# Optimization experiments

Measured on AMD Instinct MI355X. Metric: run time of the kernel, lower is better.

Reference implementation:

```python
import jax, jax.numpy as jnp
import numpy as np

SEQ_LEN = 2048
EMB = 512
BATCH = 8


def _xavier_uniform(key, shape):
    fan_in, fan_out = shape[0], shape[1]
    bound = float(np.sqrt(6.0 / (fan_in + fan_out)))
    return jax.random.uniform(key, shape, dtype=jnp.float32, minval=-bound, maxval=bound)


def setup_inputs() -> dict:
    key = jax.random.key(0)
    kx, k1, k2 = jax.random.split(key, 3)
    x = jax.random.normal(kx, (BATCH, EMB, SEQ_LEN), dtype=jnp.float32)
    weight1 = _xavier_uniform(k1, (EMB, EMB))
    weight2 = _xavier_uniform(k2, (EMB, EMB))
    return {"x": x, "weight1": weight1, "weight2": weight2}


def reference(x, weight1, weight2):
    # x: [b, e, s]
    s = x.shape[-1]
    # projections: O(b*s*e^2)
    fitnesses1 = jnp.einsum('bes,ef->bfs', x, weight1)   # [b, e, s]
    fitnesses2 = jnp.einsum('bfs,ef->bes', x, weight2)   # [b, e, s]
    # s x t interaction matrix: O(b*s^2*e)
    weight = jnp.einsum('bes,bet->bst', fitnesses1, fitnesses2)  # [b, s, t]
    # zero strictly-upper triangle (t > s), as in torch.triu(..., diagonal=1)
    mask = jnp.triu(jnp.ones((s, s), dtype=bool), k=1)
    weight = jnp.where(mask, jnp.zeros((), dtype=weight.dtype), weight)
    fitnesses = jnp.einsum('bst,bet->bes', weight, x)    # [b, e, s]
    avg_fitness = jnp.einsum('bes,bes->be', x, fitnesses)[..., None]  # [b, e, 1]
    net_fitnesses = fitnesses - avg_fitness
    x_next = x + x * net_fitnesses
    return jax.nn.relu(x_next)
```

## Files before the change

### kernel.cpp

```cpp
#include <hip/hip_runtime.h>
#include <hip/hip_bf16.h>
#include <stdint.h>


#define SEQ 2048
#define EMB 512
#define NBATCH 8

typedef unsigned short u16;
typedef __bf16 bf16x8 __attribute__((ext_vector_type(8)));
typedef float f32x4 __attribute__((ext_vector_type(4)));
typedef u16 u16x8 __attribute__((ext_vector_type(8)));

#define AS1 __attribute__((address_space(1)))
#define AS3 __attribute__((address_space(3)))

#define SBAR do { __builtin_amdgcn_sched_barrier(0); __builtin_amdgcn_s_barrier(); \
                  __builtin_amdgcn_sched_barrier(0); } while (0)
#define LGKM0 do { asm volatile("s_waitcnt lgkmcnt(0)" ::: "memory"); \
                   __builtin_amdgcn_sched_barrier(0); } while (0)

__device__ __forceinline__ u16 f2bf(float f) {
  uint32_t u = __builtin_bit_cast(uint32_t, f);
  uint32_t r = u + 0x7FFFu + ((u >> 16) & 1u);
  return (u16)(r >> 16);
}
__device__ __forceinline__ float bf2f(u16 u) {
  return __builtin_bit_cast(float, (uint32_t)u << 16);
}
__device__ __forceinline__ void gld_lds16(const void* g, void* l) {
  __builtin_amdgcn_global_load_lds((AS1 uint32_t*)g, (AS3 uint32_t*)l, 16, 0, 0);
}

__global__ __launch_bounds__(256) void prep_x_kernel(const float* __restrict__ x,
    u16* __restrict__ xb, u16* __restrict__ xbT) {
  __shared__ float tile[64][65];
  const int b = blockIdx.z;
  const int s0 = blockIdx.x * 64, e0 = blockIdx.y * 64;
  const float* xin = x + (size_t)b * EMB * SEQ;
  const int tid = threadIdx.x;
  #pragma unroll
  for (int it = 0; it < 4; ++it) {
    int idx = it * 256 + tid;
    int r = idx >> 4, c4 = idx & 15;
    float4 v = *(const float4*)(xin + (size_t)(e0 + r) * SEQ + s0 + c4 * 4);
    tile[r][c4 * 4 + 0] = v.x; tile[r][c4 * 4 + 1] = v.y;
    tile[r][c4 * 4 + 2] = v.z; tile[r][c4 * 4 + 3] = v.w;
  }
  __syncthreads();
  u16* ob = xb + (size_t)b * EMB * SEQ;
  #pragma unroll
  for (int it = 0; it < 2; ++it) {
    int idx = it * 256 + tid; int r = idx >> 3, c8 = idx & 7;
    u16x8 o;
    #pragma unroll
    for (int q = 0; q < 8; ++q) o[q] = f2bf(tile[r][c8 * 8 + q]);
    *(u16x8*)(ob + (size_t)(e0 + r) * SEQ + s0 + c8 * 8) = o;
  }
  u16* obT = xbT + (size_t)b * SEQ * EMB;
  #pragma unroll
  for (int it = 0; it < 2; ++it) {
    int idx = it * 256 + tid; int r = idx >> 3, c8 = idx & 7;
    u16x8 o;
    #pragma unroll
    for (int q = 0; q < 8; ++q) o[q] = f2bf(tile[c8 * 8 + q][r]);
    *(u16x8*)(obT + (size_t)(s0 + r) * EMB + e0 + c8 * 8) = o;
  }
}

__global__ __launch_bounds__(256) void prep_w_kernel(const float* __restrict__ W1,
    const float* __restrict__ W2, u16* __restrict__ Wcat) {
  __shared__ float tile[32][33];
  const int c0 = blockIdx.x * 32, r0 = blockIdx.y * 32;
  const int tx = threadIdx.x, ty = threadIdx.y;
  if (blockIdx.z == 0) {
    #pragma unroll
    for (int i = 0; i < 32; i += 8)
      tile[ty + i][tx] = W1[(size_t)(r0 + ty + i) * EMB + c0 + tx];
    __syncthreads();
    #pragma unroll
    for (int i = 0; i < 32; i += 8)
      Wcat[(size_t)(c0 + ty + i) * EMB + r0 + tx] = f2bf(tile[tx][ty + i]);
  } else {
    u16* W2b = Wcat + (size_t)512 * 512;
    #pragma unroll
    for (int i = 0; i < 32; i += 8)
      W2b[(size_t)(r0 + ty + i) * EMB + c0 + tx] =
          f2bf(W2[(size_t)(r0 + ty + i) * EMB + c0 + tx]);
  }
}

struct Smem {
  __align__(16) u16 A[3][4096];
  __align__(16) u16 B[3][8192];
};

template<typename PAR>
__device__ __forceinline__ void gemm_pipe(PAR par, int nk, Smem& sm, f32x4 (&acc)[4][4]) {
  const int tid = threadIdx.x, lane = tid & 63, wave = tid >> 6;
  const int wr = wave >> 2, wc = wave & 3;
  const int ar = lane & 15, asel = lane >> 4;

  auto stage = [&](int t) {
    const u16 *ga, *gb; int lda, ldb, ka, kb;
    par(t, 0, ga, lda, ka);
    par(t, 1, gb, ldb, kb);
    u16* LA = sm.A[t % 3];
    u16* LB = sm.B[t % 3];
    {
      int line = tid >> 3, cp = (tid & 7) ^ (line & 7);
      int row = line * 2 + (cp >> 2), cc = cp & 3;
      gld_lds16(ga + (size_t)row * lda + ka + cc * 8, LA + (size_t)(wave * 64) * 8);
    }
    #pragma unroll
    for (int p = 0; p < 2; ++p) {
      int idx = p * 512 + tid;
      int line = idx >> 3, cp = (idx & 7) ^ (line & 7);
      int row = line * 2 + (cp >> 2), cc = cp & 3;
      gld_lds16(gb + (size_t)row * ldb + kb + cc * 8, LB + (size_t)(p * 512 + wave * 64) * 8);
    }
  };
  auto ldfrag = [&](const u16* base, int rloc) -> bf16x8 {
    int line = rloc >> 1;
    int ch = line * 8 + ((((rloc & 1) << 2) | asel) ^ (line & 7));
    return *reinterpret_cast<const bf16x8*>(base + (size_t)ch * 8);
  };

  stage(0);
  if (nk > 1) stage(1);
  if (nk > 1) { asm volatile("s_waitcnt vmcnt(3)" ::: "memory"); }
  else        { asm volatile("s_waitcnt vmcnt(0)" ::: "memory"); }
  SBAR;

  for (int t = 0; t < nk; ++t) {
    const u16* A = sm.A[t % 3];
    const u16* B = sm.B[t % 3];
    bf16x8 af[4], bf[4];
    #pragma unroll
    for (int m = 0; m < 4; ++m) af[m] = ldfrag(A, wr * 64 + m * 16 + ar);
    #pragma unroll
    for (int n = 0; n < 4; ++n) bf[n] = ldfrag(B, wc * 64 + n * 16 + ar);
    if (t + 2 < nk) stage(t + 2);
    LGKM0;
    __builtin_amdgcn_s_setprio(1);
    #pragma unroll
    for (int m = 0; m < 4; ++m)
      #pragma unroll
      for (int n = 0; n < 4; ++n)
        acc[m][n] = __builtin_amdgcn_mfma_f32_16x16x32_bf16(af[m], bf[n], acc[m][n], 0, 0, 0);
    __builtin_amdgcn_s_setprio(0);
    if (t + 1 < nk) {
      if (t + 2 < nk) { asm volatile("s_waitcnt vmcnt(3)" ::: "memory"); }
      else            { asm volatile("s_waitcnt vmcnt(0)" ::: "memory"); }
    }
    SBAR;
  }
}

template<int MODE>
__global__ __launch_bounds__(512, 4) void k_gemm(
    const u16* __restrict__ X1, const u16* __restrict__ X2,
    const u16* __restrict__ X3, const u16* __restrict__ X4,
    u16* __restrict__ O16, u16* __restrict__ O16b) {
  __shared__ Smem sm;
  const int tid  = threadIdx.x;
  const int lane = tid & 63;
  const int wave = tid >> 6;
  const int wr = wave >> 2;
  const int wc = wave & 3;
  const int bz = blockIdx.z;
  const int id = blockIdx.x;

  f32x4 acc[4][4];
  #pragma unroll
  for (int i = 0; i < 4; ++i)
    #pragma unroll
    for (int j = 0; j < 4; ++j) acc[i][j] = (f32x4){0.f, 0.f, 0.f, 0.f};

  const int r0 = (lane >> 4) * 4;
  const int cn = lane & 15;

  if (MODE == 0) {
    const u16 *Ap, *Bp;
    int m = 0, n = 0, m2 = 0, n2 = 0;
    if (id < 64) {
      m = id & 15; n = id >> 4;
      Ap = X1 + (size_t)bz * SEQ * EMB + (size_t)(m * 128) * 512;
      Bp = X2 + (size_t)(n * 256) * 512;
    } else {
      int id2 = id - 64; m2 = id2 >> 3; n2 = id2 & 7;
      Ap = X2 + (size_t)512 * 512 + (size_t)(m2 * 128) * 512;
      Bp = X1 + (size_t)bz * SEQ * EMB + (size_t)(n2 * 256) * 512;
    }
    auto par = [&](int t, int ab, const u16*& gp, int& ld, int& k) {
      gp = ab ? Bp : Ap; ld = 512; k = t * 32;
    };
    gemm_pipe(par, 16, sm, acc);
    if (id < 64) {
      u16* C = O16 + (size_t)bz * SEQ * 1024;
      #pragma unroll
      for (int mm = 0; mm < 4; ++mm)
        #pragma unroll
        for (int nn = 0; nn < 4; ++nn)
          #pragma unroll
          for (int r = 0; r < 4; ++r) {
            int lr = wr * 64 + mm * 16 + r0 + r, lc = wc * 64 + nn * 16 + cn;
            C[(size_t)(m * 128 + lr) * 1024 + n * 256 + lc] = f2bf(acc[mm][nn][r]);
          }
    } else {
      u16* C = O16b + (size_t)bz * EMB * SEQ;
      #pragma unroll
      for (int mm = 0; mm < 4; ++mm)
        #pragma unroll
        for (int nn = 0; nn < 4; ++nn)
          #pragma unroll
          for (int r = 0; r < 4; ++r) {
            int lr = wr * 64 + mm * 16 + r0 + r, lc = wc * 64 + nn * 16 + cn;
            C[(size_t)(m2 * 128 + lr) * SEQ + n2 * 256 + lc] = f2bf(acc[mm][nn][r]);
          }
    }
  } else if (MODE == 1) {
    if (id < 16) {
      const int i = id & 7, p = id >> 3;
      const u16* Fb = X1 + (size_t)bz * SEQ * 1024;
      const u16* Ap = Fb + (size_t)(i * 256 + p * 128) * 1024;
      const u16* Bp = Fb + 512 + (size_t)(i * 256) * 1024;
      auto par = [&](int t, int ab, const u16*& gp, int& ld, int& k) {
        gp = ab ? Bp : Ap; ld = 1024; k = t * 32;
      };
      gemm_pipe(par, 16, sm, acc);
      u16* C = O16 + (size_t)(bz * 8 + i) * 256 * 256;
      #pragma unroll
      for (int mm = 0; mm < 4; ++mm)
        #pragma unroll
        for (int nn = 0; nn < 4; ++nn)
          #pragma unroll
          for (int r = 0; r < 4; ++r) {
            int lr = wr * 64 + mm * 16 + r0 + r, lc = wc * 64 + nn * 16 + cn;
            int grow = p * 128 + lr;
            float v = (lc > grow) ? 0.f : acc[mm][nn][r];
            C[(size_t)grow * 256 + lc] = f2bf(v);
          }
    } else {
      const int id2 = id - 16, j = id2 & 7, sub = id2 >> 3;
      const int m = sub >> 1, n = sub & 1;
      const u16* Ap = X2 + (size_t)bz * EMB * SEQ + (size_t)(m * 128) * SEQ + j * 256;
      const u16* Bp = X3 + (size_t)bz * EMB * SEQ + (size_t)(n * 256) * SEQ + j * 256;
      auto par = [&](int t, int ab, const u16*& gp, int& ld, int& k) {
        gp = ab ? Bp : Ap; ld = SEQ; k = t * 32;
      };
      gemm_pipe(par, 8, sm, acc);
      u16* C = O16b + (size_t)(bz * 8 + j) * EMB * EMB;
      #pragma unroll
      for (int mm = 0; mm < 4; ++mm)
        #pragma unroll
        for (int nn = 0; nn < 4; ++nn)
          #pragma unroll
          for (int r = 0; r < 4; ++r) {
            int lr = wr * 64 + mm * 16 + r0 + r, lc = wc * 64 + nn * 16 + cn;
            C[(size_t)(m * 128 + lr) * EMB + n * 256 + lc] = f2bf(acc[mm][nn][r]);
          }
    }
  } else {
    const int i = id & 7, m = id >> 3;
    const u16* Agp = (i > 0) ? X1 + (size_t)(bz * 7 + i - 1) * EMB * EMB + (size_t)(m * 128) * 512
                             : X1;
    const u16* Bf1 = X2 + (size_t)bz * SEQ * 1024 + (size_t)(i * 256) * 1024;
    const u16* Axb = X3 + (size_t)bz * EMB * SEQ + (size_t)(m * 128) * SEQ;
    const u16* Bsd = X4 + (size_t)(bz * 8 + i) * 256 * 256;
    auto par = [&](int t, int ab, const u16*& gp, int& ld, int& k) {
      int tt = (i > 0) ? t : t + 16;
      if (tt < 16) {
        if (!ab) { gp = Agp; ld = 512;  k = tt * 32; }
        else     { gp = Bf1; ld = 1024; k = tt * 32; }
      } else {
        int u = tt - 16;
        if (!ab) { gp = Axb; ld = SEQ; k = i * 256 + u * 32; }
        else     { gp = Bsd; ld = 256; k = u * 32; }
      }
    };
    gemm_pipe(par, (i > 0) ? 24 : 8, sm, acc);
    u16* C = O16 + (size_t)bz * EMB * SEQ;
    #pragma unroll
    for (int mm = 0; mm < 4; ++mm)
      #pragma unroll
      for (int nn = 0; nn < 4; ++nn)
        #pragma unroll
        for (int r = 0; r < 4; ++r) {
          int lr = wr * 64 + mm * 16 + r0 + r, lc = wc * 64 + nn * 16 + cn;
          C[(size_t)(m * 128 + lr) * SEQ + i * 256 + lc] = f2bf(acc[mm][nn][r]);
        }
  }
}

__global__ __launch_bounds__(256) void k_prefix(const u16* __restrict__ Gc,
                                                u16* __restrict__ Gp) {
  const int b = blockIdx.z;
  const size_t base = ((size_t)blockIdx.x * 256 + threadIdx.x) * 8;
  float run[8] = {0.f, 0.f, 0.f, 0.f, 0.f, 0.f, 0.f, 0.f};
  #pragma unroll
  for (int j = 0; j < 7; ++j) {
    u16x8 v = *(const u16x8*)(Gc + (size_t)(b * 8 + j) * EMB * EMB + base);
    u16x8 o;
    #pragma unroll
    for (int q = 0; q < 8; ++q) { run[q] += bf2f(v[q]); o[q] = f2bf(run[q]); }
    *(u16x8*)(Gp + (size_t)(b * 7 + j) * EMB * EMB + base) = o;
  }
}

__global__ __launch_bounds__(256) void finalize_kernel(const u16* __restrict__ xb,
    const u16* __restrict__ fitb, float* __restrict__ out) {
  const size_t row = blockIdx.x;
  const u16* xr = xb + row * SEQ;
  const u16* fr = fitb + row * SEQ;
  float* orow = out + row * SEQ;
  const int tid = threadIdx.x;

  float xv[2][4], fv[2][4];
  float part = 0.f;
  #pragma unroll
  for (int i = 0; i < 2; ++i) {
    const int s0 = i * 1024 + tid * 4;
    ushort4 xu = *reinterpret_cast<const ushort4*>(xr + s0);
    ushort4 fu = *reinterpret_cast<const ushort4*>(fr + s0);
    xv[i][0] = bf2f(xu.x); xv[i][1] = bf2f(xu.y); xv[i][2] = bf2f(xu.z); xv[i][3] = bf2f(xu.w);
    fv[i][0] = bf2f(fu.x); fv[i][1] = bf2f(fu.y); fv[i][2] = bf2f(fu.z); fv[i][3] = bf2f(fu.w);
    part += xv[i][0] * fv[i][0] + xv[i][1] * fv[i][1] + xv[i][2] * fv[i][2] + xv[i][3] * fv[i][3];
  }
  #pragma unroll
  for (int off = 1; off < 64; off <<= 1) part += __shfl_xor(part, off);
  __shared__ float wsum[4];
  const int wave = tid >> 6, lane = tid & 63;
  if (lane == 0) wsum[wave] = part;
  __syncthreads();
  const float avg = wsum[0] + wsum[1] + wsum[2] + wsum[3];

  #pragma unroll
  for (int i = 0; i < 2; ++i) {
    float4 o;
    o.x = xv[i][0] * (1.f + fv[i][0] - avg); o.x = o.x > 0.f ? o.x : 0.f;
    o.y = xv[i][1] * (1.f + fv[i][1] - avg); o.y = o.y > 0.f ? o.y : 0.f;
    o.z = xv[i][2] * (1.f + fv[i][2] - avg); o.z = o.z > 0.f ? o.z : 0.f;
    o.w = xv[i][3] * (1.f + fv[i][3] - avg); o.w = o.w > 0.f ? o.w : 0.f;
    reinterpret_cast<float4*>(orow)[i * 256 + tid] = o;
  }
}

extern "C" void kernel_launch(void* const* d_in, const int* in_sizes, int n_in,
                              void* d_out, int out_size, void* d_ws, size_t ws_size,
                              hipStream_t stream) {
  const float* x  = (const float*)d_in[0];
  const float* W1 = (const float*)d_in[1];
  const float* W2 = (const float*)d_in[2];
  float* out = (float*)d_out;

  char* ws = (char*)d_ws;
  const size_t nX = (size_t)NBATCH * EMB * SEQ;

  size_t off = 0;
  u16* xb   = (u16*)(ws + off); off += nX * 2;
  u16* Fcat = (u16*)(ws + off); off += (size_t)NBATCH * SEQ * 1024 * 2;
  const size_t offOverlay = off;
  u16* xbT  = (u16*)(ws + off); off += nX * 2;
  u16* Wcat = (u16*)(ws + off); off += (size_t)1024 * 512 * 2;
  u16* F2n  = (u16*)(ws + off); off += nX * 2;
  u16* Sd   = (u16*)(ws + off); off += (size_t)NBATCH * 8 * 256 * 256 * 2;
  u16* Gc   = (u16*)(ws + off); off += (size_t)NBATCH * 8 * EMB * EMB * 2;
  u16* Gp   = (u16*)(ws + off); off += (size_t)NBATCH * 7 * EMB * EMB * 2;
  u16* fitb = (u16*)(ws + offOverlay);

  prep_x_kernel<<<dim3(SEQ / 64, EMB / 64, NBATCH), 256, 0, stream>>>(x, xb, xbT);
  prep_w_kernel<<<dim3(16, 16, 2), dim3(32, 8), 0, stream>>>(W1, W2, Wcat);

  k_gemm<0><<<dim3(96, 1, NBATCH), 512, 0, stream>>>(
      xbT, Wcat, nullptr, nullptr, Fcat, F2n);

  k_gemm<1><<<dim3(80, 1, NBATCH), 512, 0, stream>>>(
      Fcat, xb, F2n, nullptr, Sd, Gc);

  k_prefix<<<dim3(128, 1, NBATCH), 256, 0, stream>>>(Gc, Gp);

  k_gemm<2><<<dim3(32, 1, NBATCH), 512, 0, stream>>>(
      Gp, Fcat, xb, Sd, fitb, nullptr);

  finalize_kernel<<<NBATCH * EMB, 256, 0, stream>>>(xb, fitb, out);
}
```

Baseline: 117.0 us.

## Split causal-diagonal GEMM tiles to skip masked upper-triangle work

Adds a narrower N-tile (128x128) variant of the pipelined GEMM. In MODE 1 the first diagonal 128-row block now computes only the lower-left 128x128 of the diagonal S block, skipping an all-zero region. In MODE 2 each block is split along N into two 128-wide halves, so the grid doubles to 64 blocks per batch, and the first half's diagonal-band k-loop stops after 4 steps because the rest of its Sd rows are zero. This aims to cut wasted MFMA work on masked tiles and raise occupancy, at the cost of re-reading the A operand twice in MODE 2.

Measured after the change: 116.0 us. Within noise of the previous version (-0.9%).

```diff
diff --git a/kernel.cpp b/kernel.cpp
--- a/kernel.cpp
+++ b/kernel.cpp
@@ -19,6 +19,7 @@
                   __builtin_amdgcn_sched_barrier(0); } while (0)
 #define LGKM0 do { asm volatile("s_waitcnt lgkmcnt(0)" ::: "memory"); \
                    __builtin_amdgcn_sched_barrier(0); } while (0)
+#define VMC(n) asm volatile("s_waitcnt vmcnt(" #n ")" ::: "memory")
 
 __device__ __forceinline__ u16 f2bf(float f) {
   uint32_t u = __builtin_bit_cast(uint32_t, f);
@@ -95,8 +96,8 @@
   __align__(16) u16 B[3][8192];
 };
 
-template<typename PAR>
-__device__ __forceinline__ void gemm_pipe(PAR par, int nk, Smem& sm, f32x4 (&acc)[4][4]) {
+template<int NB, typename PAR>
+__device__ __forceinline__ void gemm_pipe(PAR par, int nk, Smem& sm, f32x4 (&acc)[4][NB]) {
   const int tid = threadIdx.x, lane = tid & 63, wave = tid >> 6;
   const int wr = wave >> 2, wc = wave & 3;
   const int ar = lane & 15, asel = lane >> 4;
@@ -113,7 +114,7 @@
       gld_lds16(ga + (size_t)row * lda + ka + cc * 8, LA + (size_t)(wave * 64) * 8);
     }
     #pragma unroll
-    for (int p = 0; p < 2; ++p) {
+    for (int p = 0; p < NB / 2; ++p) {
       int idx = p * 512 + tid;
       int line = idx >> 3, cp = (idx & 7) ^ (line & 7);
       int row = line * 2 + (cp >> 2), cc = cp & 3;
@@ -128,30 +129,30 @@
 
   stage(0);
   if (nk > 1) stage(1);
-  if (nk > 1) { asm volatile("s_waitcnt vmcnt(3)" ::: "memory"); }
-  else        { asm volatile("s_waitcnt vmcnt(0)" ::: "memory"); }
+  if (nk > 1) { if constexpr (NB == 4) { VMC(3); } else { VMC(2); } }
+  else        { VMC(0); }
   SBAR;
 
   for (int t = 0; t < nk; ++t) {
     const u16* A = sm.A[t % 3];
     const u16* B = sm.B[t % 3];
-    bf16x8 af[4], bf[4];
+    bf16x8 af[4], bf[NB];
     #pragma unroll
     for (int m = 0; m < 4; ++m) af[m] = ldfrag(A, wr * 64 + m * 16 + ar);
     #pragma unroll
-    for (int n = 0; n < 4; ++n) bf[n] = ldfrag(B, wc * 64 + n * 16 + ar);
+    for (int n = 0; n < NB; ++n) bf[n] = ldfrag(B, wc * (16 * NB) + n * 16 + ar);
     if (t + 2 < nk) stage(t + 2);
     LGKM0;
     __builtin_amdgcn_s_setprio(1);
     #pragma unroll
     for (int m = 0; m < 4; ++m)
       #pragma unroll
-      for (int n = 0; n < 4; ++n)
+      for (int n = 0; n < NB; ++n)
         acc[m][n] = __builtin_amdgcn_mfma_f32_16x16x32_bf16(af[m], bf[n], acc[m][n], 0, 0, 0);
     __builtin_amdgcn_s_setprio(0);
     if (t + 1 < nk) {
-      if (t + 2 < nk) { asm volatile("s_waitcnt vmcnt(3)" ::: "memory"); }
-      else            { asm volatile("s_waitcnt vmcnt(0)" ::: "memory"); }
+      if (t + 2 < nk) { if constexpr (NB == 4) { VMC(3); } else { VMC(2); } }
+      else            { VMC(0); }
     }
     SBAR;
   }
@@ -171,12 +172,6 @@
   const int bz = blockIdx.z;
   const int id = blockIdx.x;
 
-  f32x4 acc[4][4];
-  #pragma unroll
-  for (int i = 0; i < 4; ++i)
-    #pragma unroll
-    for (int j = 0; j < 4; ++j) acc[i][j] = (f32x4){0.f, 0.f, 0.f, 0.f};
-
   const int r0 = (lane >> 4) * 4;
   const int cn = lane & 15;
 
@@ -195,7 +190,12 @@
     auto par = [&](int t, int ab, const u16*& gp, int& ld, int& k) {
       gp = ab ? Bp : Ap; ld = 512; k = t * 32;
     };
-    gemm_pipe(par, 16, sm, acc);
+    f32x4 acc[4][4];
+    #pragma unroll
+    for (int i = 0; i < 4; ++i)
+      #pragma unroll
+      for (int j = 0; j < 4; ++j) acc[i][j] = (f32x4){0.f, 0.f, 0.f, 0.f};
+    gemm_pipe<4>(par, 16, sm, acc);
     if (id < 64) {
       u16* C = O16 + (size_t)bz * SEQ * 1024;
       #pragma unroll
@@ -220,15 +220,45 @@
           }
     }
   } else if (MODE == 1) {
-    if (id < 16) {
-      const int i = id & 7, p = id >> 3;
+    if (id < 8) {
+      const int i = id;
       const u16* Fb = X1 + (size_t)bz * SEQ * 1024;
-      const u16* Ap = Fb + (size_t)(i * 256 + p * 128) * 1024;
+      const u16* Ap = Fb + (size_t)(i * 256) * 1024;
       const u16* Bp = Fb + 512 + (size_t)(i * 256) * 1024;
       auto par = [&](int t, int ab, const u16*& gp, int& ld, int& k) {
         gp = ab ? Bp : Ap; ld = 1024; k = t * 32;
       };
-      gemm_pipe(par, 16, sm, acc);
+      f32x4 acc[4][2];
+      #pragma unroll
+      for (int a = 0; a < 4; ++a)
+        #pragma unroll
+        for (int b = 0; b < 2; ++b) acc[a][b] = (f32x4){0.f, 0.f, 0.f, 0.f};
+      gemm_pipe<2>(par, 16, sm, acc);
+      u16* C = O16 + (size_t)(bz * 8 + i) * 256 * 256;
+      #pragma unroll
+      for (int mm = 0; mm < 4; ++mm)
+        #pragma unroll
+        for (int nn = 0; nn < 2; ++nn)
+          #pragma unroll
+          for (int r = 0; r < 4; ++r) {
+            int lr = wr * 64 + mm * 16 + r0 + r, lc = wc * 32 + nn * 16 + cn;
+            float v = (lc > lr) ? 0.f : acc[mm][nn][r];
+            C[(size_t)lr * 256 + lc] = f2bf(v);
+          }
+    } else if (id < 16) {
+      const int i = id - 8;
+      const u16* Fb = X1 + (size_t)bz * SEQ * 1024;
+      const u16* Ap = Fb + (size_t)(i * 256 + 128) * 1024;
+      const u16* Bp = Fb + 512 + (size_t)(i * 256) * 1024;
+      auto par = [&](int t, int ab, const u16*& gp, int& ld, int& k) {
+        gp = ab ? Bp : Ap; ld = 1024; k = t * 32;
+      };
+      f32x4 acc[4][4];
+      #pragma unroll
+      for (int a = 0; a < 4; ++a)
+        #pragma unroll
+        for (int b = 0; b < 4; ++b) acc[a][b] = (f32x4){0.f, 0.f, 0.f, 0.f};
+      gemm_pipe<4>(par, 16, sm, acc);
       u16* C = O16 + (size_t)(bz * 8 + i) * 256 * 256;
       #pragma unroll
       for (int mm = 0; mm < 4; ++mm)
@@ -237,7 +267,7 @@
           #pragma unroll
           for (int r = 0; r < 4; ++r) {
             int lr = wr * 64 + mm * 16 + r0 + r, lc = wc * 64 + nn * 16 + cn;
-            int grow = p * 128 + lr;
+            int grow = 128 + lr;
             float v = (lc > grow) ? 0.f : acc[mm][nn][r];
             C[(size_t)grow * 256 + lc] = f2bf(v);
           }
@@ -249,7 +279,12 @@
       auto par = [&](int t, int ab, const u16*& gp, int& ld, int& k) {
         gp = ab ? Bp : Ap; ld = SEQ; k = t * 32;
       };
-      gemm_pipe(par, 8, sm, acc);
+      f32x4 acc[4][4];
+      #pragma unroll
+      for (int a = 0; a < 4; ++a)
+        #pragma unroll
+        for (int b = 0; b < 4; ++b) acc[a][b] = (f32x4){0.f, 0.f, 0.f, 0.f};
+      gemm_pipe<4>(par, 8, sm, acc);
       u16* C = O16b + (size_t)(bz * 8 + j) * EMB * EMB;
       #pragma unroll
       for (int mm = 0; mm < 4; ++mm)
@@ -262,12 +297,12 @@
           }
     }
   } else {
-    const int i = id & 7, m = id >> 3;
+    const int i = id & 7, m = (id >> 3) & 3, n2 = id >> 5;
     const u16* Agp = (i > 0) ? X1 + (size_t)(bz * 7 + i - 1) * EMB * EMB + (size_t)(m * 128) * 512
                              : X1;
-    const u16* Bf1 = X2 + (size_t)bz * SEQ * 1024 + (size_t)(i * 256) * 1024;
+    const u16* Bf1 = X2 + (size_t)bz * SEQ * 1024 + (size_t)(i * 256 + n2 * 128) * 1024;
     const u16* Axb = X3 + (size_t)bz * EMB * SEQ + (size_t)(m * 128) * SEQ;
-    const u16* Bsd = X4 + (size_t)(bz * 8 + i) * 256 * 256;
+    const u16* Bsd = X4 + (size_t)(bz * 8 + i) * 256 * 256 + (size_t)(n2 * 128) * 256;
     auto par = [&](int t, int ab, const u16*& gp, int& ld, int& k) {
       int tt = (i > 0) ? t : t + 16;
       if (tt < 16) {
@@ -279,16 +314,22 @@
         else     { gp = Bsd; ld = 256; k = u * 32; }
       }
     };
-    gemm_pipe(par, (i > 0) ? 24 : 8, sm, acc);
+    const int nkd = n2 ? 8 : 4;
+    f32x4 acc[4][2];
+    #pragma unroll
+    for (int a = 0; a < 4; ++a)
+      #pragma unroll
+      for (int b = 0; b < 2; ++b) acc[a][b] = (f32x4){0.f, 0.f, 0.f, 0.f};
+    gemm_pipe<2>(par, (i > 0 ? 16 : 0) + nkd, sm, acc);
     u16* C = O16 + (size_t)bz * EMB * SEQ;
     #pragma unroll
     for (int mm = 0; mm < 4; ++mm)
       #pragma unroll
-      for (int nn = 0; nn < 4; ++nn)
+      for (int nn = 0; nn < 2; ++nn)
         #pragma unroll
         for (int r = 0; r < 4; ++r) {
-          int lr = wr * 64 + mm * 16 + r0 + r, lc = wc * 64 + nn * 16 + cn;
-          C[(size_t)(m * 128 + lr) * SEQ + i * 256 + lc] = f2bf(acc[mm][nn][r]);
+          int lr = wr * 64 + mm * 16 + r0 + r, lc = wc * 32 + nn * 16 + cn;
+          C[(size_t)(m * 128 + lr) * SEQ + i * 256 + n2 * 128 + lc] = f2bf(acc[mm][nn][r]);
         }
   }
 }
@@ -380,7 +421,7 @@
 
   k_prefix<<<dim3(128, 1, NBATCH), 256, 0, stream>>>(Gc, Gp);
 
-  k_gemm<2><<<dim3(32, 1, NBATCH), 512, 0, stream>>>(
+  k_gemm<2><<<dim3(64, 1, NBATCH), 512, 0, stream>>>(
       Gp, Fcat, xb, Sd, fitb, nullptr);
 
   finalize_kernel<<<NBATCH * EMB, 256, 0, stream>>>(xb, fitb, out);
```
